# Optimization experiments

Measured on AMD Instinct MI355X. Metric: run time of the kernel, lower is better.

The kernel has to match this reference:

```python
import jax, jax.numpy as jnp
import numpy as np
from jax import lax


def ternary_quant(w):
    # Layer-wise ternary quantization: alpha = mean(|w|), threshold = 0.001*alpha
    alpha = lax.stop_gradient(jnp.mean(jnp.abs(w)))
    thr = 0.001 * alpha
    q = jnp.where(w > thr, 1.0, jnp.where(w < -thr, -1.0, 0.0))
    return alpha * q


def setup_inputs() -> dict:
    key = jax.random.key(0)
    k1, k2, k3, k4, k5 = jax.random.split(key, 5)
    B, C, H, W = 32, 384, 64, 64
    fan_in = C * 3 * 3
    bound = 1.0 / np.sqrt(fan_in)  # torch Conv2d default init scale
    return {
        "x": jax.random.normal(k1, (B, C, H, W), dtype=jnp.float32),
        "weight": jax.random.uniform(k2, (C, C, 3, 3), dtype=jnp.float32, minval=-bound, maxval=bound),
        "bias": jax.random.uniform(k3, (C,), dtype=jnp.float32, minval=-bound, maxval=bound),
        "time_emb": jax.random.normal(k4, (B, 512), dtype=jnp.float32),
        "y": jax.random.randint(k5, (B,), 0, 1000, dtype=jnp.int64),
    }


def reference(x, weight, bias, time_emb, y):
    # time_emb and y are accepted but unused, matching Downsample.forward
    qw = ternary_quant(weight)
    out = lax.conv_general_dilated(
        x, qw,
        window_strides=(2, 2),
        padding=((1, 1), (1, 1)),
        dimension_numbers=("NCHW", "OIHW", "NCHW"),
    )
    return out + bias[None, :, None, None]
```

## Files before the change

### kernel.cpp

```cpp
#include <hip/hip_runtime.h>
#include <hip/hip_bf16.h>


#define CIN   384
#define HIN   64
#define WIN   64
#define OHW   32
#define KDIM  3456
#define NWELT 1327104
#define MDIM  32768
#define NT    54

using bf16 = __hip_bfloat16;
typedef __attribute__((ext_vector_type(8))) short short8;
typedef __attribute__((ext_vector_type(4))) float floatx4;
typedef __attribute__((ext_vector_type(2))) unsigned short ushort2v;

#define AS1 __attribute__((address_space(1)))
#define AS3 __attribute__((address_space(3)))
#define DMA16(g, l) __builtin_amdgcn_global_load_lds((const AS1 void*)(g), (AS3 void*)(l), 16, 0, 0)

#define EDGE_V(N) do { \
    asm volatile("s_waitcnt vmcnt(" #N ")" ::: "memory"); \
    __builtin_amdgcn_s_barrier(); \
    __builtin_amdgcn_sched_barrier(0); \
} while (0)
#define EDGE_VL(N) do { \
    asm volatile("s_waitcnt vmcnt(" #N ")" ::: "memory"); \
    asm volatile("s_waitcnt lgkmcnt(0)" ::: "memory"); \
    __builtin_amdgcn_s_barrier(); \
    __builtin_amdgcn_sched_barrier(0); \
} while (0)

#define MFMA_Q(ACCR, ACCC, BF) do { \
    __builtin_amdgcn_s_setprio(1); \
    _Pragma("unroll") \
    for (int ks = 0; ks < 2; ++ks) \
        _Pragma("unroll") \
        for (int fo = 0; fo < 3; ++fo) \
            _Pragma("unroll") \
            for (int fm = 0; fm < 2; ++fm) \
                acc[(ACCR) + fo][(ACCC) + fm] = __builtin_amdgcn_mfma_f32_16x16x32_bf16( \
                    af[ks][fo], BF[ks][fm], acc[(ACCR) + fo][(ACCC) + fm], 0, 0, 0); \
    __builtin_amdgcn_s_setprio(0); \
} while (0)

#define NPART  62
#define ZG_F   16
#define XN_OFF 256
#define WQ_OFF (256 + 100663296)

__global__ void absum_part(const float* __restrict__ w, float* __restrict__ ws) {
    const float4* w4 = (const float4*)w;
    float s = 0.f;
    for (int i = blockIdx.x * 256 + threadIdx.x; i < NWELT / 4; i += NPART * 256) {
        float4 v = w4[i];
        s += fabsf(v.x) + fabsf(v.y) + fabsf(v.z) + fabsf(v.w);
    }
    for (int off = 32; off; off >>= 1) s += __shfl_down(s, off, 64);
    __shared__ float red[4];
    if ((threadIdx.x & 63) == 0) red[threadIdx.x >> 6] = s;
    __syncthreads();
    if (threadIdx.x == 0) ws[2 + blockIdx.x] = red[0] + red[1] + red[2] + red[3];
}

__global__ void absum_final(float* __restrict__ ws) {
    if (threadIdx.x == 0) {
        float s = 0.f;
        for (int i = 0; i < NPART; ++i) s += ws[2 + i];
        float alpha = s * (1.0f / NWELT);
        ws[0] = alpha;
        ws[1] = 1e-3f * alpha;
        ws[ZG_F + 0] = 0.f; ws[ZG_F + 1] = 0.f;
        ws[ZG_F + 2] = 0.f; ws[ZG_F + 3] = 0.f;
    }
}

__global__ void quant_kernel(const float* __restrict__ w, const float* __restrict__ ws,
                             bf16* __restrict__ wq) {
    int j = blockIdx.x * 256 + threadIdx.x;
    if (j >= NWELT) return;
    float thr = ws[1];
    int o = j / KDIM;
    int rmd = j - o * KDIM;
    int khkw = rmd / 384;
    int c = rmd - khkw * 384;
    float v = w[((o * 384 + c) * 9) + khkw];
    float q = (v > thr) ? 1.f : ((v < -thr) ? -1.f : 0.f);
    wq[j] = __float2bfloat16(q);
}

__global__ void nhwc_kernel(const float* __restrict__ x, bf16* __restrict__ xn) {
    int nh = blockIdx.x;
    int n = nh >> 6, h = nh & 63;
    int c0 = blockIdx.y * 64;
    __shared__ bf16 tile[64][66];
    const float* src = x + ((n * CIN + c0) * HIN + h) * WIN;
    for (int i = 0; i < 4; ++i) {
        int s = threadIdx.x + i * 256;
        int cl = s >> 4, w4 = (s & 15) * 4;
        float4 v = *(const float4*)(src + cl * 4096 + w4);
        bf16 t0[2], t1[2];
        t0[0] = __float2bfloat16(v.x); t0[1] = __float2bfloat16(v.y);
        t1[0] = __float2bfloat16(v.z); t1[1] = __float2bfloat16(v.w);
        *(ushort2v*)&tile[cl][w4]     = *(ushort2v*)t0;
        *(ushort2v*)&tile[cl][w4 + 2] = *(ushort2v*)t1;
    }
    __syncthreads();
    bf16* dst = xn + ((size_t)(n * HIN + h) * WIN) * CIN + c0;
    for (int i = 0; i < 2; ++i) {
        int q = threadIdx.x + i * 256;
        int wc = q >> 3, c8 = (q & 7) * 8;
        bf16 tmp[8];
        #pragma unroll
        for (int j = 0; j < 8; ++j) tmp[j] = tile[c8 + j][wc];
        *(short8*)(dst + (size_t)wc * CIN + c8) = *(short8*)tmp;
    }
}

#define BM  128

__global__ __launch_bounds__(512, 2) void conv_gemm(const bf16* __restrict__ xn,
                                                    const bf16* __restrict__ wq,
                                                    const float* __restrict__ ws,
                                                    const float* __restrict__ bias,
                                                    float* __restrict__ out,
                                                    const bf16* __restrict__ zg) {
    __shared__ __align__(16) bf16 lW[2][384 * 64];
    __shared__ __align__(16) bf16 lX[3][128 * 64];
    const int m_base = blockIdx.x * BM;
    const int tid = threadIdx.x;
    const int lane = tid & 63;
    const int wv = tid >> 6;
    const int io = wv & 3;
    const int im = wv >> 2;
    const int g = (lane & 7) ^ (lane >> 3);

    const bf16* pw[2][3];
    int wLoff[2][3];
    #pragma unroll
    for (int h = 0; h < 2; ++h)
        #pragma unroll
        for (int j = 0; j < 3; ++j) {
            int rr = h * 192 + wv * 24 + j * 8;
            pw[h][j] = wq + (size_t)(rr + (lane >> 3)) * KDIM + g * 8;
            wLoff[h][j] = rr * 64;
        }

    const bf16* pxn[2];
    int oh2[2], ow2[2], xLoff[2];
    #pragma unroll
    for (int h = 0; h < 2; ++h) {
        int rr = h * 64 + wv * 8;
        int m = m_base + rr + (lane >> 3);
        int n = m >> 10, oh = (m >> 5) & 31, ow = m & 31;
        pxn[h] = xn + (size_t)n * (HIN * WIN * CIN) + g * 8;
        oh2[h] = 2 * oh - 1;
        ow2[h] = 2 * ow - 1;
        xLoff[h] = rr * 64;
    }

    const int l15 = lane & 15, quad = lane >> 4, l7 = lane & 7;
    const int octA = (quad ^ l7) * 8;
    const int octB = ((4 + quad) ^ l7) * 8;
    int aoff[2][3], boff[2][2];
    #pragma unroll
    for (int h = 0; h < 2; ++h)
        #pragma unroll
        for (int fo = 0; fo < 3; ++fo)
            aoff[h][fo] = (h * 192 + io * 48 + fo * 16 + l15) * 64;
    #pragma unroll
    for (int h = 0; h < 2; ++h)
        #pragma unroll
        for (int fm = 0; fm < 2; ++fm)
            boff[h][fm] = (h * 64 + im * 32 + fm * 16 + l15) * 64;

    floatx4 acc[6][4];
    #pragma unroll
    for (int i = 0; i < 6; ++i)
        #pragma unroll
        for (int j = 0; j < 4; ++j)
            acc[i][j] = (floatx4){0.f, 0.f, 0.f, 0.f};

    {
        #pragma unroll
        for (int h = 0; h < 2; ++h) {
            int ih = oh2[h], iw = ow2[h];
            const bf16* p = (ih >= 0 && iw >= 0) ? pxn[h] + (ih * WIN + iw) * CIN : zg;
            DMA16(p, &lX[0][xLoff[h]]);
        }
        #pragma unroll
        for (int h = 0; h < 2; ++h)
            #pragma unroll
            for (int j = 0; j < 3; ++j) DMA16(pw[h][j], &lW[0][wLoff[h][j]]);
        #pragma unroll
        for (int h = 0; h < 2; ++h) {
            int ih = oh2[h], iw = ow2[h];
            const bf16* p = (ih >= 0 && iw >= 0) ? pxn[h] + (ih * WIN + iw) * CIN + 64 : zg;
            DMA16(p, &lX[1][xLoff[h]]);
        }
        EDGE_V(2);
    }

    short8 af[2][3], bfl[2][2], bfh[2][2];

    for (int t = 0; t < NT - 1; ++t) {
        bf16* lWc = lW[t & 1];
        const int x_cur = t % 3;
        bf16* lWn = lW[(t + 1) & 1];
        bf16* lXn2 = lX[(t + 2) % 3];
        const int kW = (t + 1) * 64;
        const int s2 = t + 2;
        const int khkw2 = s2 / 6, cc2 = s2 - khkw2 * 6;
        const int kh2 = khkw2 / 3, kw2 = khkw2 - kh2 * 3;

        #pragma unroll
        for (int fo = 0; fo < 3; ++fo) {
            af[0][fo] = *(const short8*)(lWc + aoff[0][fo] + octA);
            af[1][fo] = *(const short8*)(lWc + aoff[0][fo] + octB);
        }
        #pragma unroll
        for (int fm = 0; fm < 2; ++fm) {
            bfl[0][fm] = *(const short8*)(lX[x_cur] + boff[0][fm] + octA);
            bfl[1][fm] = *(const short8*)(lX[x_cur] + boff[0][fm] + octB);
        }
        #pragma unroll
        for (int h = 0; h < 2; ++h)
            #pragma unroll
            for (int j = 0; j < 3; ++j) DMA16(pw[h][j] + kW, lWn + wLoff[h][j]);
        MFMA_Q(0, 0, bfl);

        #pragma unroll
        for (int fm = 0; fm < 2; ++fm) {
            bfh[0][fm] = *(const short8*)(lX[x_cur] + boff[1][fm] + octA);
            bfh[1][fm] = *(const short8*)(lX[x_cur] + boff[1][fm] + octB);
        }
        #pragma unroll
        for (int h = 0; h < 2; ++h) {
            int ih = oh2[h] + kh2, iw = ow2[h] + kw2;
            bool valid = (ih >= 0) & (iw >= 0) & (s2 < NT);
            const bf16* p = valid ? pxn[h] + (ih * WIN + iw) * CIN + cc2 * 64 : zg;
            DMA16(p, lXn2 + xLoff[h]);
        }
        EDGE_V(8);
        MFMA_Q(0, 2, bfh);

        #pragma unroll
        for (int fo = 0; fo < 3; ++fo) {
            af[0][fo] = *(const short8*)(lWc + aoff[1][fo] + octA);
            af[1][fo] = *(const short8*)(lWc + aoff[1][fo] + octB);
        }
        MFMA_Q(3, 2, bfh);

        EDGE_VL(2);
        MFMA_Q(3, 0, bfl);
    }

    {
        bf16* lWc = lW[1];
        bf16* lXc = lX[53 % 3];
        #pragma unroll
        for (int fo = 0; fo < 3; ++fo) {
            af[0][fo] = *(const short8*)(lWc + aoff[0][fo] + octA);
            af[1][fo] = *(const short8*)(lWc + aoff[0][fo] + octB);
        }
        #pragma unroll
        for (int fm = 0; fm < 2; ++fm) {
            bfl[0][fm] = *(const short8*)(lXc + boff[0][fm] + octA);
            bfl[1][fm] = *(const short8*)(lXc + boff[0][fm] + octB);
        }
        MFMA_Q(0, 0, bfl);
        #pragma unroll
        for (int fm = 0; fm < 2; ++fm) {
            bfh[0][fm] = *(const short8*)(lXc + boff[1][fm] + octA);
            bfh[1][fm] = *(const short8*)(lXc + boff[1][fm] + octB);
        }
        MFMA_Q(0, 2, bfh);
        #pragma unroll
        for (int fo = 0; fo < 3; ++fo) {
            af[0][fo] = *(const short8*)(lWc + aoff[1][fo] + octA);
            af[1][fo] = *(const short8*)(lWc + aoff[1][fo] + octB);
        }
        MFMA_Q(3, 2, bfh);
        MFMA_Q(3, 0, bfl);
    }

    float alpha = ws[0];
    #pragma unroll
    for (int i = 0; i < 6; ++i) {
        int o0 = (i / 3) * 192 + io * 48 + (i % 3) * 16 + quad * 4;
        #pragma unroll
        for (int j = 0; j < 4; ++j) {
            int m = m_base + (j >> 1) * 64 + im * 32 + (j & 1) * 16 + l15;
            int nn = m >> 10, ohh = (m >> 5) & 31, oww = m & 31;
            #pragma unroll
            for (int r = 0; r < 4; ++r) {
                int o = o0 + r;
                out[((nn * 384 + o) * OHW + ohh) * OHW + oww] = alpha * acc[i][j][r] + bias[o];
            }
        }
    }
}

extern "C" void kernel_launch(void* const* d_in, const int* in_sizes, int n_in,
                              void* d_out, int out_size, void* d_ws, size_t ws_size,
                              hipStream_t stream) {
    (void)in_sizes; (void)n_in; (void)out_size; (void)ws_size;
    const float* x    = (const float*)d_in[0];
    const float* w    = (const float*)d_in[1];
    const float* bias = (const float*)d_in[2];
    float* out = (float*)d_out;
    float* wsf = (float*)d_ws;
    bf16* xn = (bf16*)((char*)d_ws + XN_OFF);
    bf16* wq = (bf16*)((char*)d_ws + WQ_OFF);
    const bf16* zg = (const bf16*)(wsf + ZG_F);

    absum_part<<<NPART, 256, 0, stream>>>(w, wsf);
    absum_final<<<1, 64, 0, stream>>>(wsf);
    quant_kernel<<<(NWELT + 255) / 256, 256, 0, stream>>>(w, wsf, wq);
    nhwc_kernel<<<dim3(2048, 6), 256, 0, stream>>>(x, xn);
    conv_gemm<<<dim3(MDIM / BM, 1), 512, 0, stream>>>(xn, wq, wsf, bias, out, zg);
}
```

Measured before the change: 437.5 us.

## Switch conv GEMM to 32x32x16 MFMA with contiguous warp tiles and one barrier per step

Replaces the 16x16x32 bf16 MFMA tiling with 32x32x16 MFMAs. Each warp now owns a contiguous 96x64 output block held in 3x2 floatx16 accumulators, with LDS fragment reads rewritten as byte offsets under the same XOR swizzle. The main loop is reorganised to read fragments in four k-chunks interleaved with MFMAs, and the two barriers per K-step collapse into a single vmcnt wait plus barrier at the end. The aim is fewer LDS fragment reads and fewer MFMA issues per FLOP, plus less synchronisation stall. The trade-off is less overlap granularity and heavier reliance on the single barrier for buffer-reuse safety.

```diff
diff --git a/kernel.cpp b/kernel.cpp
--- a/kernel.cpp
+++ b/kernel.cpp
@@ -13,7 +13,7 @@
 
 using bf16 = __hip_bfloat16;
 typedef __attribute__((ext_vector_type(8))) short short8;
-typedef __attribute__((ext_vector_type(4))) float floatx4;
+typedef __attribute__((ext_vector_type(16))) float floatx16;
 typedef __attribute__((ext_vector_type(2))) unsigned short ushort2v;
 
 #define AS1 __attribute__((address_space(1)))
@@ -24,25 +24,6 @@
     asm volatile("s_waitcnt vmcnt(" #N ")" ::: "memory"); \
     __builtin_amdgcn_s_barrier(); \
     __builtin_amdgcn_sched_barrier(0); \
-} while (0)
-#define EDGE_VL(N) do { \
-    asm volatile("s_waitcnt vmcnt(" #N ")" ::: "memory"); \
-    asm volatile("s_waitcnt lgkmcnt(0)" ::: "memory"); \
-    __builtin_amdgcn_s_barrier(); \
-    __builtin_amdgcn_sched_barrier(0); \
-} while (0)
-
-#define MFMA_Q(ACCR, ACCC, BF) do { \
-    __builtin_amdgcn_s_setprio(1); \
-    _Pragma("unroll") \
-    for (int ks = 0; ks < 2; ++ks) \
-        _Pragma("unroll") \
-        for (int fo = 0; fo < 3; ++fo) \
-            _Pragma("unroll") \
-            for (int fm = 0; fm < 2; ++fm) \
-                acc[(ACCR) + fo][(ACCC) + fm] = __builtin_amdgcn_mfma_f32_16x16x32_bf16( \
-                    af[ks][fo], BF[ks][fm], acc[(ACCR) + fo][(ACCC) + fm], 0, 0, 0); \
-    __builtin_amdgcn_s_setprio(0); \
 } while (0)
 
 #define NPART  62
@@ -160,27 +141,22 @@
         xLoff[h] = rr * 64;
     }
 
-    const int l15 = lane & 15, quad = lane >> 4, l7 = lane & 7;
-    const int octA = (quad ^ l7) * 8;
-    const int octB = ((4 + quad) ^ l7) * 8;
-    int aoff[2][3], boff[2][2];
-    #pragma unroll
-    for (int h = 0; h < 2; ++h)
-        #pragma unroll
-        for (int fo = 0; fo < 3; ++fo)
-            aoff[h][fo] = (h * 192 + io * 48 + fo * 16 + l15) * 64;
-    #pragma unroll
-    for (int h = 0; h < 2; ++h)
-        #pragma unroll
-        for (int fm = 0; fm < 2; ++fm)
-            boff[h][fm] = (h * 64 + im * 32 + fm * 16 + l15) * 64;
-
-    floatx4 acc[6][4];
-    #pragma unroll
-    for (int i = 0; i < 6; ++i)
-        #pragma unroll
-        for (int j = 0; j < 4; ++j)
-            acc[i][j] = (floatx4){0.f, 0.f, 0.f, 0.f};
+    const int l31 = lane & 31, hi = lane >> 5, l7 = lane & 7;
+    int abase[3], bbase[2], octoff[4];
+    #pragma unroll
+    for (int fo = 0; fo < 3; ++fo) abase[fo] = (io * 96 + fo * 32 + l31) * 128;
+    #pragma unroll
+    for (int fm = 0; fm < 2; ++fm) bbase[fm] = (im * 64 + fm * 32 + l31) * 128;
+    #pragma unroll
+    for (int c = 0; c < 4; ++c) octoff[c] = ((c * 2 + hi) ^ l7) * 16;
+
+    floatx16 acc[3][2];
+    #pragma unroll
+    for (int i = 0; i < 3; ++i)
+        #pragma unroll
+        for (int j = 0; j < 2; ++j)
+            #pragma unroll
+            for (int r = 0; r < 16; ++r) acc[i][j][r] = 0.f;
 
     {
         #pragma unroll
@@ -202,11 +178,31 @@
         EDGE_V(2);
     }
 
-    short8 af[2][3], bfl[2][2], bfh[2][2];
+    short8 afr[2][3], bfr[2][2];
+
+#define READC(CB, C) do { \
+    _Pragma("unroll") \
+    for (int fo = 0; fo < 3; ++fo) \
+        afr[CB][fo] = *(const short8*)((const char*)lWc + abase[fo] + octoff[C]); \
+    _Pragma("unroll") \
+    for (int fm = 0; fm < 2; ++fm) \
+        bfr[CB][fm] = *(const short8*)((const char*)lXc + bbase[fm] + octoff[C]); \
+} while (0)
+
+#define MFMAC(CB) do { \
+    __builtin_amdgcn_s_setprio(1); \
+    _Pragma("unroll") \
+    for (int fo = 0; fo < 3; ++fo) \
+        _Pragma("unroll") \
+        for (int fm = 0; fm < 2; ++fm) \
+            acc[fo][fm] = __builtin_amdgcn_mfma_f32_32x32x16_bf16( \
+                afr[CB][fo], bfr[CB][fm], acc[fo][fm], 0, 0, 0); \
+    __builtin_amdgcn_s_setprio(0); \
+} while (0)
 
     for (int t = 0; t < NT - 1; ++t) {
-        bf16* lWc = lW[t & 1];
-        const int x_cur = t % 3;
+        const bf16* lWc = lW[t & 1];
+        const bf16* lXc = lX[t % 3];
         bf16* lWn = lW[(t + 1) & 1];
         bf16* lXn2 = lX[(t + 2) % 3];
         const int kW = (t + 1) * 64;
@@ -214,27 +210,12 @@
         const int khkw2 = s2 / 6, cc2 = s2 - khkw2 * 6;
         const int kh2 = khkw2 / 3, kw2 = khkw2 - kh2 * 3;
 
-        #pragma unroll
-        for (int fo = 0; fo < 3; ++fo) {
-            af[0][fo] = *(const short8*)(lWc + aoff[0][fo] + octA);
-            af[1][fo] = *(const short8*)(lWc + aoff[0][fo] + octB);
-        }
-        #pragma unroll
-        for (int fm = 0; fm < 2; ++fm) {
-            bfl[0][fm] = *(const short8*)(lX[x_cur] + boff[0][fm] + octA);
-            bfl[1][fm] = *(const short8*)(lX[x_cur] + boff[0][fm] + octB);
-        }
+        READC(0, 0);
+        READC(1, 1);
         #pragma unroll
         for (int h = 0; h < 2; ++h)
             #pragma unroll
             for (int j = 0; j < 3; ++j) DMA16(pw[h][j] + kW, lWn + wLoff[h][j]);
-        MFMA_Q(0, 0, bfl);
-
-        #pragma unroll
-        for (int fm = 0; fm < 2; ++fm) {
-            bfh[0][fm] = *(const short8*)(lX[x_cur] + boff[1][fm] + octA);
-            bfh[1][fm] = *(const short8*)(lX[x_cur] + boff[1][fm] + octB);
-        }
         #pragma unroll
         for (int h = 0; h < 2; ++h) {
             int ih = oh2[h] + kh2, iw = ow2[h] + kw2;
@@ -242,61 +223,39 @@
             const bf16* p = valid ? pxn[h] + (ih * WIN + iw) * CIN + cc2 * 64 : zg;
             DMA16(p, lXn2 + xLoff[h]);
         }
-        EDGE_V(8);
-        MFMA_Q(0, 2, bfh);
-
-        #pragma unroll
-        for (int fo = 0; fo < 3; ++fo) {
-            af[0][fo] = *(const short8*)(lWc + aoff[1][fo] + octA);
-            af[1][fo] = *(const short8*)(lWc + aoff[1][fo] + octB);
-        }
-        MFMA_Q(3, 2, bfh);
-
-        EDGE_VL(2);
-        MFMA_Q(3, 0, bfl);
+        MFMAC(0);
+        READC(0, 2);
+        MFMAC(1);
+        READC(1, 3);
+        MFMAC(0);
+        MFMAC(1);
+        EDGE_V(2);
     }
 
     {
-        bf16* lWc = lW[1];
-        bf16* lXc = lX[53 % 3];
-        #pragma unroll
-        for (int fo = 0; fo < 3; ++fo) {
-            af[0][fo] = *(const short8*)(lWc + aoff[0][fo] + octA);
-            af[1][fo] = *(const short8*)(lWc + aoff[0][fo] + octB);
-        }
+        const bf16* lWc = lW[1];
+        const bf16* lXc = lX[53 % 3];
+        READC(0, 0);
+        READC(1, 1);
+        MFMAC(0);
+        READC(0, 2);
+        MFMAC(1);
+        READC(1, 3);
+        MFMAC(0);
+        MFMAC(1);
+    }
+
+    float alpha = ws[0];
+    #pragma unroll
+    for (int fo = 0; fo < 3; ++fo) {
         #pragma unroll
         for (int fm = 0; fm < 2; ++fm) {
-            bfl[0][fm] = *(const short8*)(lXc + boff[0][fm] + octA);
-            bfl[1][fm] = *(const short8*)(lXc + boff[0][fm] + octB);
-        }
-        MFMA_Q(0, 0, bfl);
-        #pragma unroll
-        for (int fm = 0; fm < 2; ++fm) {
-            bfh[0][fm] = *(const short8*)(lXc + boff[1][fm] + octA);
-            bfh[1][fm] = *(const short8*)(lXc + boff[1][fm] + octB);
-        }
-        MFMA_Q(0, 2, bfh);
-        #pragma unroll
-        for (int fo = 0; fo < 3; ++fo) {
-            af[0][fo] = *(const short8*)(lWc + aoff[1][fo] + octA);
-            af[1][fo] = *(const short8*)(lWc + aoff[1][fo] + octB);
-        }
-        MFMA_Q(3, 2, bfh);
-        MFMA_Q(3, 0, bfl);
-    }
-
-    float alpha = ws[0];
-    #pragma unroll
-    for (int i = 0; i < 6; ++i) {
-        int o0 = (i / 3) * 192 + io * 48 + (i % 3) * 16 + quad * 4;
-        #pragma unroll
-        for (int j = 0; j < 4; ++j) {
-            int m = m_base + (j >> 1) * 64 + im * 32 + (j & 1) * 16 + l15;
+            int m = m_base + im * 64 + fm * 32 + l31;
             int nn = m >> 10, ohh = (m >> 5) & 31, oww = m & 31;
             #pragma unroll
-            for (int r = 0; r < 4; ++r) {
-                int o = o0 + r;
-                out[((nn * 384 + o) * OHW + ohh) * OHW + oww] = alpha * acc[i][j][r] + bias[o];
+            for (int r = 0; r < 16; ++r) {
+                int o = io * 96 + fo * 32 + (r & 3) + 8 * (r >> 2) + 4 * hi;
+                out[((nn * 384 + o) * OHW + ohh) * OHW + oww] = alpha * acc[fo][fm][r] + bias[o];
             }
         }
     }
```

After: 442.5 us. No clear change (+1.2%).
